# Optimization experiments

Measured on AMD Instinct MI355X. Metric: run time of the kernel, lower is better.

## Reference

```python
import jax, jax.numpy as jnp
import numpy as np

N_QUBITS = 4
STATE_DIM = 2 ** N_QUBITS  # 16


def _angle_embed_state(angles):
    """PennyLane AngleEmbedding with RX rotations applied to |0...0>.

    RX(t)|0> = cos(t/2)|0> - i sin(t/2)|1>; the full state is the tensor
    product of the per-qubit 2-vectors. angles: [..., N_QUBITS] real.
    Returns complex64 state of shape [..., 2**N_QUBITS].
    """
    half = angles * 0.5
    a0 = jnp.cos(half).astype(jnp.complex64)           # amplitude of |0>
    a1 = (-1j) * jnp.sin(half).astype(jnp.complex64)   # amplitude of |1>
    amps = jnp.stack([a0, a1], axis=-1)                # [..., n, 2]
    psi = jnp.einsum('...i,...j,...k,...l->...ijkl',
                     amps[..., 0, :], amps[..., 1, :],
                     amps[..., 2, :], amps[..., 3, :])
    return psi.reshape(angles.shape[:-1] + (STATE_DIM,))


def setup_inputs() -> dict:
    key = jax.random.key(0)
    ks = jax.random.split(key, 5)
    B, D = 65536, 1024
    features = jax.random.normal(ks[0], (B, D), dtype=jnp.float32)
    W_proj = jax.random.normal(ks[1], (N_QUBITS, D), dtype=jnp.float32) / np.sqrt(D)
    b_proj = jnp.zeros((N_QUBITS,), dtype=jnp.float32)
    ref_vec = jax.random.normal(ks[2], (N_QUBITS,), dtype=jnp.float32)
    W_cls = jax.random.normal(ks[3], (1, 1), dtype=jnp.float32)
    b_cls = jnp.zeros((1,), dtype=jnp.float32)
    return {"features": features, "W_proj": W_proj, "b_proj": b_proj,
            "ref_vec": ref_vec, "W_cls": W_cls, "b_cls": b_cls}


def reference(features, W_proj, b_proj, ref_vec, W_cls, b_cls):
    # feature_projector: Linear(1024, n_qubits) + Tanh
    q_inputs = jnp.tanh(features @ W_proj.T + b_proj)          # [B, n]
    # reference state from tanh(reference_vector)
    ref_state = _angle_embed_state(jnp.tanh(ref_vec))          # [16]
    # batched quantum states (replaces the per-sample Python loop)
    psi = _angle_embed_state(q_inputs)                          # [B, 16]
    # fidelity = |vdot(psi, ref)|^2 = |sum conj(psi)*ref|^2
    overlap = jnp.einsum('bs,s->b', jnp.conj(psi), ref_state)  # [B] complex
    fidelity = (jnp.abs(overlap) ** 2).astype(jnp.float32)     # [B]
    kernel_outputs = fidelity[:, None]                          # [B, 1]
    return kernel_outputs @ W_cls.T + b_cls                     # [B, 1]
```

## Files before the change

### kernel.cpp

```cpp
#include <hip/hip_runtime.h>
#include <math.h>

#define DIMF 1024

__global__ __launch_bounds__(256) void qkc_kernel(
    const float* __restrict__ features,
    const float* __restrict__ W_proj,
    const float* __restrict__ b_proj,
    const float* __restrict__ ref_vec,
    const float* __restrict__ W_cls,
    const float* __restrict__ b_cls,
    float* __restrict__ out,
    int nrows)
{
    const int lane = threadIdx.x & 63;
    const int wib  = threadIdx.x >> 6;
    const int wpb  = blockDim.x >> 6;
    const int gwave  = blockIdx.x * wpb + wib;
    const int nwaves = gridDim.x * wpb;

    float4 w[4][4];
    #pragma unroll
    for (int q = 0; q < 4; ++q)
        #pragma unroll
        for (int k = 0; k < 4; ++k)
            w[q][k] = *reinterpret_cast<const float4*>(
                &W_proj[q * DIMF + k * 256 + lane * 4]);

    float u[4], bp[4];
    #pragma unroll
    for (int q = 0; q < 4; ++q) {
        u[q]  = tanhf(ref_vec[q]);
        bp[q] = b_proj[q];
    }
    const float wc = W_cls[0];
    const float bc = b_cls[0];

    for (int row = gwave; row < nrows; row += nwaves) {
        const float* frow = features + (size_t)row * DIMF;
        float4 f[4];
        #pragma unroll
        for (int k = 0; k < 4; ++k)
            f[k] = *reinterpret_cast<const float4*>(&frow[k * 256 + lane * 4]);

        float acc[4];
        #pragma unroll
        for (int q = 0; q < 4; ++q) {
            float s = f[0].x * w[q][0].x + f[0].y * w[q][0].y
                    + f[0].z * w[q][0].z + f[0].w * w[q][0].w;
            #pragma unroll
            for (int k = 1; k < 4; ++k)
                s += f[k].x * w[q][k].x + f[k].y * w[q][k].y
                   + f[k].z * w[q][k].z + f[k].w * w[q][k].w;
            #pragma unroll
            for (int off = 32; off >= 1; off >>= 1)
                s += __shfl_xor(s, off, 64);
            acc[q] = s;
        }

        if (lane == 0) {
            float fid = 1.0f;
            #pragma unroll
            for (int q = 0; q < 4; ++q) {
                float t = tanhf(acc[q] + bp[q]);
                float c = cosf((t - u[q]) * 0.5f);
                fid *= c * c;
            }
            out[row] = fid * wc + bc;
        }
    }
}

extern "C" void kernel_launch(void* const* d_in, const int* in_sizes, int n_in,
                              void* d_out, int out_size, void* d_ws, size_t ws_size,
                              hipStream_t stream) {
    const float* features = (const float*)d_in[0];
    const float* W_proj   = (const float*)d_in[1];
    const float* b_proj   = (const float*)d_in[2];
    const float* ref_vec  = (const float*)d_in[3];
    const float* W_cls    = (const float*)d_in[4];
    const float* b_cls    = (const float*)d_in[5];
    float* out = (float*)d_out;

    const int nrows = out_size;
    const int block = 256;
    const int wpb = block / 64;
    int blocks = (nrows + wpb - 1) / wpb;
    if (blocks > 2048) blocks = 2048;

    qkc_kernel<<<blocks, block, 0, stream>>>(
        features, W_proj, b_proj, ref_vec, W_cls, b_cls, out, nrows);
}
```

Baseline: 363.1 us.

## Unroll fixed rows per wave with lane-parallel epilogue and fast math

```diff
diff --git a/kernel.cpp b/kernel.cpp
--- a/kernel.cpp
+++ b/kernel.cpp
@@ -2,8 +2,14 @@
 #include <math.h>
 
 #define DIMF 1024
+#define RPW  8
 
-__global__ __launch_bounds__(256) void qkc_kernel(
+__device__ __forceinline__ float fast_tanh(float x) {
+    float e = __expf(2.0f * x);
+    return 1.0f - __fdividef(2.0f, e + 1.0f);
+}
+
+__global__ __launch_bounds__(256, 4) void qkc_kernel(
     const float* __restrict__ features,
     const float* __restrict__ W_proj,
     const float* __restrict__ b_proj,
@@ -11,13 +17,11 @@
     const float* __restrict__ W_cls,
     const float* __restrict__ b_cls,
     float* __restrict__ out,
-    int nrows)
+    int nrows, int nwaves)
 {
-    const int lane = threadIdx.x & 63;
-    const int wib  = threadIdx.x >> 6;
-    const int wpb  = blockDim.x >> 6;
-    const int gwave  = blockIdx.x * wpb + wib;
-    const int nwaves = gridDim.x * wpb;
+    const int lane  = threadIdx.x & 63;
+    const int wib   = threadIdx.x >> 6;
+    const int gwave = blockIdx.x * (blockDim.x >> 6) + wib;
 
     float4 w[4][4];
     #pragma unroll
@@ -30,45 +34,52 @@
     float u[4], bp[4];
     #pragma unroll
     for (int q = 0; q < 4; ++q) {
-        u[q]  = tanhf(ref_vec[q]);
+        u[q]  = fast_tanh(ref_vec[q]);
         bp[q] = b_proj[q];
     }
     const float wc = W_cls[0];
     const float bc = b_cls[0];
 
-    for (int row = gwave; row < nrows; row += nwaves) {
-        const float* frow = features + (size_t)row * DIMF;
-        float4 f[4];
-        #pragma unroll
-        for (int k = 0; k < 4; ++k)
-            f[k] = *reinterpret_cast<const float4*>(&frow[k * 256 + lane * 4]);
+    float e[4] = {0.f, 0.f, 0.f, 0.f};
 
-        float acc[4];
-        #pragma unroll
-        for (int q = 0; q < 4; ++q) {
-            float s = f[0].x * w[q][0].x + f[0].y * w[q][0].y
-                    + f[0].z * w[q][0].z + f[0].w * w[q][0].w;
-            #pragma unroll
-            for (int k = 1; k < 4; ++k)
-                s += f[k].x * w[q][k].x + f[k].y * w[q][k].y
-                   + f[k].z * w[q][k].z + f[k].w * w[q][k].w;
-            #pragma unroll
-            for (int off = 32; off >= 1; off >>= 1)
-                s += __shfl_xor(s, off, 64);
-            acc[q] = s;
-        }
+    #pragma unroll
+    for (int i = 0; i < RPW; ++i) {
+        const int row = gwave + i * nwaves;
+        if (row < nrows) {
+            const float* frow = features + (size_t)row * DIMF;
+            float4 f0 = *reinterpret_cast<const float4*>(&frow[        lane * 4]);
+            float4 f1 = *reinterpret_cast<const float4*>(&frow[256  +  lane * 4]);
+            float4 f2 = *reinterpret_cast<const float4*>(&frow[512  +  lane * 4]);
+            float4 f3 = *reinterpret_cast<const float4*>(&frow[768  +  lane * 4]);
 
-        if (lane == 0) {
-            float fid = 1.0f;
             #pragma unroll
             for (int q = 0; q < 4; ++q) {
-                float t = tanhf(acc[q] + bp[q]);
-                float c = cosf((t - u[q]) * 0.5f);
-                fid *= c * c;
+                float s = f0.x * w[q][0].x + f0.y * w[q][0].y
+                        + f0.z * w[q][0].z + f0.w * w[q][0].w
+                        + f1.x * w[q][1].x + f1.y * w[q][1].y
+                        + f1.z * w[q][1].z + f1.w * w[q][1].w
+                        + f2.x * w[q][2].x + f2.y * w[q][2].y
+                        + f2.z * w[q][2].z + f2.w * w[q][2].w
+                        + f3.x * w[q][3].x + f3.y * w[q][3].y
+                        + f3.z * w[q][3].z + f3.w * w[q][3].w;
+                #pragma unroll
+                for (int off = 32; off >= 1; off >>= 1)
+                    s += __shfl_xor(s, off, 64);
+                if (lane == i) e[q] = s;
             }
-            out[row] = fid * wc + bc;
         }
     }
+
+    float fid = 1.0f;
+    #pragma unroll
+    for (int q = 0; q < 4; ++q) {
+        float t = fast_tanh(e[q] + bp[q]);
+        float c = __cosf(t - u[q]);
+        fid *= 0.5f * (1.0f + c);
+    }
+    const int orow = gwave + lane * nwaves;
+    if (lane < RPW && orow < nrows)
+        out[orow] = fid * wc + bc;
 }
 
 extern "C" void kernel_launch(void* const* d_in, const int* in_sizes, int n_in,
@@ -84,10 +95,11 @@
 
     const int nrows = out_size;
     const int block = 256;
-    const int wpb = block / 64;
-    int blocks = (nrows + wpb - 1) / wpb;
-    if (blocks > 2048) blocks = 2048;
+    const int wpb   = block / 64;
+    const int target_waves = (nrows + RPW - 1) / RPW;
+    int blocks = (target_waves + wpb - 1) / wpb;
+    const int nwaves = blocks * wpb;
 
     qkc_kernel<<<blocks, block, 0, stream>>>(
-        features, W_proj, b_proj, ref_vec, W_cls, b_cls, out, nrows);
+        features, W_proj, b_proj, ref_vec, W_cls, b_cls, out, nrows, nwaves);
 }
```

Result: no change. 362.8 us (-0.1%).
